# Kernel tuning notes

Hardware: AMD Instinct MI355X
Metric: run time of the kernel (lower is better)

Reference implementation:

```python
import jax, jax.numpy as jnp
import numpy as np

B, S, D = 4, 2048, 1024
H, DK, DV, DOUT = 16, 64, 64, 1024
NEG = -1.0e9


def setup_inputs() -> dict:
    key = jax.random.key(0)
    ks = jax.random.split(key, 12)
    sq = lambda fan_in: 1.0 / np.sqrt(fan_in)
    return {
        "query": jax.random.normal(ks[0], (B, S, D), jnp.float32),
        "key": jax.random.normal(ks[1], (B, S, D), jnp.float32),
        "value": jax.random.normal(ks[2], (B, S, D), jnp.float32),
        "attention_mask": jax.random.randint(ks[3], (B, 1, 1, S), 0, 2, jnp.int32),
        "wq": jax.random.normal(ks[4], (D, H * DK), jnp.float32) * sq(D),
        "bq": jnp.zeros((H * DK,), jnp.float32),
        "wk": jax.random.normal(ks[5], (D, H * DK), jnp.float32) * sq(D),
        "bk": jnp.zeros((H * DK,), jnp.float32),
        "wv": jax.random.normal(ks[6], (D, H * DV), jnp.float32) * sq(D),
        "bv": jnp.zeros((H * DV,), jnp.float32),
        "wo": jax.random.normal(ks[7], (H * DV, DOUT), jnp.float32) * sq(H * DV),
        "bo": jnp.zeros((DOUT,), jnp.float32),
    }


def _split_heads(x, head_dim):
    b, s, _ = x.shape
    return x.reshape(b, s, H, head_dim).transpose(0, 2, 1, 3)  # [B,H,S,hd]


def reference(query, key, value, attention_mask, wq, bq, wk, bk, wv, bv, wo, bo):
    q = _split_heads(query @ wq + bq, DK)   # [B,H,S,DK]
    k = _split_heads(key @ wk + bk, DK)     # [B,H,S,DK]
    v = _split_heads(value @ wv + bv, DV)   # [B,H,S,DV]
    logits = jnp.einsum("bhqd,bhkd->bhqk", q, k) / jnp.sqrt(jnp.float32(DK))
    logits = logits + attention_mask.astype(logits.dtype) * NEG
    attn = jax.nn.softmax(logits, axis=-1)
    out = jnp.einsum("bhqk,bhkd->bhqd", attn, v)          # [B,H,S,DV]
    out = out.transpose(0, 2, 1, 3).reshape(query.shape[0], -1, H * DV)
    return out @ wo + bo
```

## Files before the change

kernel.cpp:

```cpp
#include <hip/hip_runtime.h>
#include <hip/hip_bf16.h>
#include <math.h>

#define Bv 4
#define Sv 2048
#define Dv 1024
#define Hv 16
#define HD 64
#define NEGV (-1.0e9f)

typedef __attribute__((ext_vector_type(8))) short bf16x8;
typedef __attribute__((ext_vector_type(4))) short s16x4;
typedef __attribute__((ext_vector_type(4))) float f32x4;

__device__ __forceinline__ short f2bf(float f) {
    union { __hip_bfloat16 h; short s; } u;
    u.h = __float2bfloat16(f);
    return u.s;
}

__device__ __forceinline__ void glds16(const void* g, void* l) {
    __builtin_amdgcn_global_load_lds(
        (const __attribute__((address_space(1))) void*)g,
        (__attribute__((address_space(3))) void*)l, 16, 0, 0);
}

__global__ __launch_bounds__(256) void cvt_bf16(const float* __restrict__ X,
                                                unsigned short* __restrict__ Y) {
    const size_t i = ((size_t)blockIdx.x * 256 + threadIdx.x) * 8;
    const float4 a = *(const float4*)&X[i];
    const float4 b = *(const float4*)&X[i + 4];
    bf16x8 o = {f2bf(a.x), f2bf(a.y), f2bf(a.z), f2bf(a.w),
                f2bf(b.x), f2bf(b.y), f2bf(b.z), f2bf(b.w)};
    *(bf16x8*)&Y[i] = o;
}

__global__ __launch_bounds__(256) void transpose_w(const float* __restrict__ W,
                                                   unsigned short* __restrict__ WT) {
    __shared__ float T[64][65];
    const int t = threadIdx.x;
    const int n0 = blockIdx.x * 64, k0 = blockIdx.y * 64;
    #pragma unroll
    for (int i = 0; i < 4; ++i) {
        const int k = (t >> 4) + 16 * i;
        const int nc = (t & 15) * 4;
        const float4 v = *(const float4*)&W[(size_t)(k0 + k) * 1024 + n0 + nc];
        T[k][nc + 0] = v.x; T[k][nc + 1] = v.y;
        T[k][nc + 2] = v.z; T[k][nc + 3] = v.w;
    }
    __syncthreads();
    const int n = t >> 2, kc = (t & 3) * 16;
    #pragma unroll
    for (int j4 = 0; j4 < 4; ++j4) {
        s16x4 o;
        #pragma unroll
        for (int jj = 0; jj < 4; ++jj) o[jj] = f2bf(T[kc + j4 * 4 + jj][n]);
        *(s16x4*)&WT[(size_t)(n0 + n) * 1024 + k0 + kc + j4 * 4] = o;
    }
}

__global__ __launch_bounds__(256) void transpose_v(const unsigned short* __restrict__ Vin,
                                                   unsigned short* __restrict__ VT) {
    __shared__ unsigned short T[64][72];
    const int t = threadIdx.x;
    const int s0 = blockIdx.x * 64;
    const int bh = blockIdx.y;
    const size_t ib = (size_t)bh * Sv * 64;
    const size_t ob = (size_t)bh * 64 * Sv;
    {
        const int s = t >> 2, dc = (t & 3) * 16;
        const bf16x8 a = *(const bf16x8*)&Vin[ib + (size_t)(s0 + s) * 64 + dc];
        const bf16x8 b = *(const bf16x8*)&Vin[ib + (size_t)(s0 + s) * 64 + dc + 8];
        *(bf16x8*)&T[s][dc] = a;
        *(bf16x8*)&T[s][dc + 8] = b;
    }
    __syncthreads();
    const int dv = t >> 2, sc = (t & 3) * 16;
    #pragma unroll
    for (int j4 = 0; j4 < 4; ++j4) {
        s16x4 o;
        #pragma unroll
        for (int jj = 0; jj < 4; ++jj) o[jj] = (short)T[sc + j4 * 4 + jj][dv];
        *(s16x4*)&VT[ob + (size_t)dv * Sv + s0 + sc + j4 * 4] = o;
    }
}

template <int PERM>
__global__ __launch_bounds__(256) void gemm_mfma(const unsigned short* __restrict__ X,
                                                 const unsigned short* __restrict__ WT,
                                                 const float* __restrict__ bias,
                                                 void* __restrict__ Cv,
                                                 int M, int N, int K) {
    __shared__ short As[128 * 32];
    __shared__ short Bs[128 * 32];

    const int t = threadIdx.x;
    const int lane = t & 63, w = t >> 6;
    const int l15 = lane & 15, quad = lane >> 4;
    const int m0 = blockIdx.y * 128, n0 = blockIdx.x * 128;
    const int wm = (w >> 1) * 64, wn = (w & 1) * 64;

    f32x4 acc[4][4];
    #pragma unroll
    for (int mi = 0; mi < 4; ++mi)
        #pragma unroll
        for (int ni = 0; ni < 4; ++ni) acc[mi][ni] = (f32x4){0.f, 0.f, 0.f, 0.f};

    const int srow = lane >> 2;
    const int skc = (lane & 3) * 8;

    for (int k0 = 0; k0 < K; k0 += 32) {
        #pragma unroll
        for (int i = 0; i < 2; ++i) {
            const int seg = w * 2 + i;
            const int row = seg * 16 + srow;
            glds16(&WT[(size_t)(n0 + row) * K + k0 + skc], &Bs[seg * 512]);
            glds16(&X[(size_t)(m0 + row) * K + k0 + skc], &As[seg * 512]);
        }
        __syncthreads();

        bf16x8 afr[4], bfr[4];
        #pragma unroll
        for (int mi = 0; mi < 4; ++mi)
            afr[mi] = *(const bf16x8*)&As[(wm + mi * 16 + l15) * 32 + quad * 8];
        #pragma unroll
        for (int ni = 0; ni < 4; ++ni)
            bfr[ni] = *(const bf16x8*)&Bs[(wn + ni * 16 + l15) * 32 + quad * 8];
        #pragma unroll
        for (int mi = 0; mi < 4; ++mi)
            #pragma unroll
            for (int ni = 0; ni < 4; ++ni)
                acc[mi][ni] = __builtin_amdgcn_mfma_f32_16x16x32_bf16(
                    afr[mi], bfr[ni], acc[mi][ni], 0, 0, 0);
        __syncthreads();
    }

    #pragma unroll
    for (int mi = 0; mi < 4; ++mi) {
        #pragma unroll
        for (int ni = 0; ni < 4; ++ni) {
            const int col = n0 + wn + ni * 16 + l15;
            const float bsv = bias[col];
            #pragma unroll
            for (int r = 0; r < 4; ++r) {
                const int row = m0 + wm + mi * 16 + quad * 4 + r;
                const float vv = acc[mi][ni][r] + bsv;
                if constexpr (PERM == 0) {
                    ((float*)Cv)[(size_t)row * N + col] = vv;
                } else {
                    const int bb = row / Sv, s = row % Sv;
                    const int hh = col >> 6, d = col & 63;
                    ((unsigned short*)Cv)[((((size_t)bb * Hv + hh) * Sv + s) << 6) + d] =
                        (unsigned short)f2bf(vv);
                }
            }
        }
    }
}

__global__ __launch_bounds__(256) void attn_mfma(const unsigned short* __restrict__ Q,
                                                 const unsigned short* __restrict__ Kg,
                                                 const unsigned short* __restrict__ VT,
                                                 const int* __restrict__ mask,
                                                 unsigned short* __restrict__ O) {
    __shared__ short Kl[64 * 72];
    __shared__ short Vl[64 * 72];
    __shared__ short Sl[128 * 72];
    __shared__ float Mk[64];

    const int t = threadIdx.x;
    const int lane = t & 63, w = t >> 6;
    const int l15 = lane & 15, quad = lane >> 4;
    const int q0 = blockIdx.x * 128;
    const int h = blockIdx.y, b = blockIdx.z;
    const int bh = b * Hv + h;
    const size_t kvb = (size_t)bh * Sv * 64;
    const size_t vtb = (size_t)bh * 64 * Sv;

    bf16x8 qf[2][2];
    #pragma unroll
    for (int ni = 0; ni < 2; ++ni) {
        const size_t qa = kvb + (size_t)(q0 + w * 32 + ni * 16 + l15) * 64 + quad * 8;
        qf[ni][0] = *(const bf16x8*)&Q[qa];
        qf[ni][1] = *(const bf16x8*)&Q[qa + 32];
    }

    float l_acc[2] = {0.f, 0.f};
    f32x4 oacc[2][4];
    #pragma unroll
    for (int mi = 0; mi < 2; ++mi)
        #pragma unroll
        for (int ni = 0; ni < 4; ++ni) oacc[mi][ni] = (f32x4){0.f, 0.f, 0.f, 0.f};

    const int srow = t >> 2, sch = (t & 3) * 16;

    for (int k0 = 0; k0 < Sv; k0 += 64) {
        __syncthreads();
        {
            const unsigned short* Ks = Kg + kvb + (size_t)k0 * 64;
            const bf16x8 a = *(const bf16x8*)&Ks[(size_t)srow * 64 + sch];
            const bf16x8 c = *(const bf16x8*)&Ks[(size_t)srow * 64 + sch + 8];
            *(bf16x8*)&Kl[srow * 72 + sch] = a;
            *(bf16x8*)&Kl[srow * 72 + sch + 8] = c;
            const unsigned short* Vs = VT + vtb + k0;
            const bf16x8 d = *(const bf16x8*)&Vs[(size_t)srow * Sv + sch];
            const bf16x8 e = *(const bf16x8*)&Vs[(size_t)srow * Sv + sch + 8];
            *(bf16x8*)&Vl[srow * 72 + sch] = d;
            *(bf16x8*)&Vl[srow * 72 + sch + 8] = e;
        }
        if (t < 64) Mk[t] = NEGV * (float)mask[(size_t)b * Sv + k0 + t];
        __syncthreads();

        #pragma unroll
        for (int mi = 0; mi < 4; ++mi) {
            const bf16x8 kf0 = *(const bf16x8*)&Kl[(mi * 16 + l15) * 72 + quad * 8];
            const bf16x8 kf1 = *(const bf16x8*)&Kl[(mi * 16 + l15) * 72 + 32 + quad * 8];
            const float4 mk4 = *(const float4*)&Mk[mi * 16 + quad * 4];
            #pragma unroll
            for (int ni = 0; ni < 2; ++ni) {
                f32x4 st = (f32x4){0.f, 0.f, 0.f, 0.f};
                st = __builtin_amdgcn_mfma_f32_16x16x32_bf16(kf0, qf[ni][0], st, 0, 0, 0);
                st = __builtin_amdgcn_mfma_f32_16x16x32_bf16(kf1, qf[ni][1], st, 0, 0, 0);
                const float p0 = __expf(st[0] * 0.125f + mk4.x);
                const float p1 = __expf(st[1] * 0.125f + mk4.y);
                const float p2 = __expf(st[2] * 0.125f + mk4.z);
                const float p3 = __expf(st[3] * 0.125f + mk4.w);
                l_acc[ni] += (p0 + p1) + (p2 + p3);
                s16x4 pv = {f2bf(p0), f2bf(p1), f2bf(p2), f2bf(p3)};
                *(s16x4*)&Sl[(w * 32 + ni * 16 + l15) * 72 + mi * 16 + quad * 4] = pv;
            }
        }

        #pragma unroll
        for (int mi = 0; mi < 2; ++mi) {
            const bf16x8 pf0 = *(const bf16x8*)&Sl[(w * 32 + mi * 16 + l15) * 72 + quad * 8];
            const bf16x8 pf1 = *(const bf16x8*)&Sl[(w * 32 + mi * 16 + l15) * 72 + 32 + quad * 8];
            #pragma unroll
            for (int ni = 0; ni < 4; ++ni) {
                const bf16x8 vf0 = *(const bf16x8*)&Vl[(ni * 16 + l15) * 72 + quad * 8];
                const bf16x8 vf1 = *(const bf16x8*)&Vl[(ni * 16 + l15) * 72 + 32 + quad * 8];
                oacc[mi][ni] = __builtin_amdgcn_mfma_f32_16x16x32_bf16(pf0, vf0, oacc[mi][ni], 0, 0, 0);
                oacc[mi][ni] = __builtin_amdgcn_mfma_f32_16x16x32_bf16(pf1, vf1, oacc[mi][ni], 0, 0, 0);
            }
        }
    }

    #pragma unroll
    for (int mi = 0; mi < 2; ++mi) {
        float l = l_acc[mi];
        l += __shfl_xor(l, 16);
        l += __shfl_xor(l, 32);
        #pragma unroll
        for (int r = 0; r < 4; ++r) {
            const float lr = __shfl(l, quad * 4 + r, 64);
            const float inv = 1.0f / lr;
            const size_t row = (size_t)b * Sv + q0 + w * 32 + mi * 16 + quad * 4 + r;
            #pragma unroll
            for (int ni = 0; ni < 4; ++ni) {
                O[row * (Hv * HD) + h * HD + ni * 16 + l15] =
                    (unsigned short)f2bf(oacc[mi][ni][r] * inv);
            }
        }
    }
}

extern "C" void kernel_launch(void* const* d_in, const int* in_sizes, int n_in,
                              void* d_out, int out_size, void* d_ws, size_t ws_size,
                              hipStream_t stream) {
    const float* query = (const float*)d_in[0];
    const float* key   = (const float*)d_in[1];
    const float* value = (const float*)d_in[2];
    const int*   amask = (const int*)d_in[3];
    const float* wq = (const float*)d_in[4];
    const float* bq = (const float*)d_in[5];
    const float* wk = (const float*)d_in[6];
    const float* bk = (const float*)d_in[7];
    const float* wv = (const float*)d_in[8];
    const float* bv = (const float*)d_in[9];
    const float* wo = (const float*)d_in[10];
    const float* bo = (const float*)d_in[11];
    float* out = (float*)d_out;

    unsigned short* wsp = (unsigned short*)d_ws;
    dim3 bb(256), gt(16, 16);

    if (ws_size >= (size_t)64 * 1024 * 1024) {
        const size_t PBQ = (size_t)Bv * Hv * Sv * HD;
        unsigned short* qb = wsp;
        unsigned short* kb = qb + PBQ;
        unsigned short* vb = kb + PBQ;
        unsigned short* ab = vb + PBQ;
        unsigned short* wt_kb = kb;
        unsigned short* wt_out = (unsigned short*)d_out;
        unsigned short* wt_vb = vb;

        const int M = Bv * Sv;
        dim3 gg(8, M / 128), gc(M * 1024 / 2048);

        cvt_bf16<<<gc, bb, 0, stream>>>(value, ab);
        transpose_w<<<gt, bb, 0, stream>>>(wv, wt_kb);
        gemm_mfma<1><<<gg, bb, 0, stream>>>(ab, wt_kb, bv, qb, M, 1024, 1024);
        transpose_v<<<dim3(Sv / 64, Bv * Hv), bb, 0, stream>>>(qb, vb);

        cvt_bf16<<<gc, bb, 0, stream>>>(query, ab);
        transpose_w<<<gt, bb, 0, stream>>>(wq, wt_kb);
        gemm_mfma<1><<<gg, bb, 0, stream>>>(ab, wt_kb, bq, qb, M, 1024, 1024);

        cvt_bf16<<<gc, bb, 0, stream>>>(key, ab);
        transpose_w<<<gt, bb, 0, stream>>>(wk, wt_out);
        gemm_mfma<1><<<gg, bb, 0, stream>>>(ab, wt_out, bk, kb, M, 1024, 1024);

        attn_mfma<<<dim3(Sv / 128, Hv, Bv), bb, 0, stream>>>(qb, kb, vb, amask, ab);

        transpose_w<<<gt, bb, 0, stream>>>(wo, wt_vb);
        gemm_mfma<0><<<gg, bb, 0, stream>>>(ab, wt_vb, bo, out, M, 1024, 1024);
    } else {
        const size_t PQ = (size_t)Hv * Sv * HD;
        unsigned short* qb = wsp;
        unsigned short* kb = qb + PQ;
        unsigned short* vb = kb + PQ;
        unsigned short* ab = vb + PQ;
        const int M = Sv;
        dim3 gg(8, M / 128), gc(M * 1024 / 2048);
        for (int b = 0; b < Bv; ++b) {
            const size_t xoff = (size_t)b * Sv * Dv;
            unsigned short* wt_kb = kb;
            unsigned short* wt_out = (unsigned short*)(out + xoff);
            unsigned short* wt_vb = vb;

            cvt_bf16<<<gc, bb, 0, stream>>>(value + xoff, ab);
            transpose_w<<<gt, bb, 0, stream>>>(wv, wt_kb);
            gemm_mfma<1><<<gg, bb, 0, stream>>>(ab, wt_kb, bv, qb, M, 1024, 1024);
            transpose_v<<<dim3(Sv / 64, Hv), bb, 0, stream>>>(qb, vb);

            cvt_bf16<<<gc, bb, 0, stream>>>(query + xoff, ab);
            transpose_w<<<gt, bb, 0, stream>>>(wq, wt_kb);
            gemm_mfma<1><<<gg, bb, 0, stream>>>(ab, wt_kb, bq, qb, M, 1024, 1024);

            cvt_bf16<<<gc, bb, 0, stream>>>(key + xoff, ab);
            transpose_w<<<gt, bb, 0, stream>>>(wk, wt_out);
            gemm_mfma<1><<<gg, bb, 0, stream>>>(ab, wt_out, bk, kb, M, 1024, 1024);

            attn_mfma<<<dim3(Sv / 128, Hv, 1), bb, 0, stream>>>(qb, kb, vb,
                                                                amask + (size_t)b * Sv, ab);

            transpose_w<<<gt, bb, 0, stream>>>(wo, wt_vb);
            gemm_mfma<0><<<gg, bb, 0, stream>>>(ab, wt_vb, bo, out + xoff, M, 1024, 1024);
        }
    }
}
```

Before: 412.1 us.

## Register-prefetch next K/V/mask tile and use exp2 with folded scale in attention

The attention kernel now loads the next K, V and mask tile into registers right after the barrier, so the global-load latency overlaps the current tile's MFMA and softmax work. The softmax exponent uses a hardware exp2 with the 1/sqrt(dk)*log2(e) scale and the mask constant folded into a single FMA. The V fragments are hoisted out of the inner loop so each is read from LDS once. A launch-bounds occupancy hint of four blocks is added. The prefetch registers add register pressure, which the occupancy hint may conflict with.

```diff
diff --git a/kernel.cpp b/kernel.cpp
--- a/kernel.cpp
+++ b/kernel.cpp
@@ -18,6 +18,12 @@
     u.h = __float2bfloat16(f);
     return u.s;
 }
+
+#if __has_builtin(__builtin_amdgcn_exp2f)
+#define EXP2F(x) __builtin_amdgcn_exp2f(x)
+#else
+#define EXP2F(x) __expf((x) * 0.6931471805599453f)
+#endif
 
 __device__ __forceinline__ void glds16(const void* g, void* l) {
     __builtin_amdgcn_global_load_lds(
@@ -158,11 +164,11 @@
     }
 }
 
-__global__ __launch_bounds__(256) void attn_mfma(const unsigned short* __restrict__ Q,
-                                                 const unsigned short* __restrict__ Kg,
-                                                 const unsigned short* __restrict__ VT,
-                                                 const int* __restrict__ mask,
-                                                 unsigned short* __restrict__ O) {
+__global__ __launch_bounds__(256, 4) void attn_mfma(const unsigned short* __restrict__ Q,
+                                                    const unsigned short* __restrict__ Kg,
+                                                    const unsigned short* __restrict__ VT,
+                                                    const int* __restrict__ mask,
+                                                    unsigned short* __restrict__ O) {
     __shared__ short Kl[64 * 72];
     __shared__ short Vl[64 * 72];
     __shared__ short Sl[128 * 72];
@@ -193,23 +199,35 @@
         for (int ni = 0; ni < 4; ++ni) oacc[mi][ni] = (f32x4){0.f, 0.f, 0.f, 0.f};
 
     const int srow = t >> 2, sch = (t & 3) * 16;
+    const unsigned short* Kst = Kg + kvb + (size_t)srow * 64 + sch;
+    const unsigned short* Vst = VT + vtb + (size_t)srow * Sv + sch;
+    const int* Mst = mask + (size_t)b * Sv;
+
+    bf16x8 kr0 = *(const bf16x8*)&Kst[0];
+    bf16x8 kr1 = *(const bf16x8*)&Kst[8];
+    bf16x8 vr0 = *(const bf16x8*)&Vst[0];
+    bf16x8 vr1 = *(const bf16x8*)&Vst[8];
+    int mreg = (t < 64) ? Mst[t] : 0;
+
+    constexpr float CS = 0.18033688011112042f;
+    constexpr float CM = NEGV * 1.4426950408889634f;
 
     for (int k0 = 0; k0 < Sv; k0 += 64) {
         __syncthreads();
-        {
-            const unsigned short* Ks = Kg + kvb + (size_t)k0 * 64;
-            const bf16x8 a = *(const bf16x8*)&Ks[(size_t)srow * 64 + sch];
-            const bf16x8 c = *(const bf16x8*)&Ks[(size_t)srow * 64 + sch + 8];
-            *(bf16x8*)&Kl[srow * 72 + sch] = a;
-            *(bf16x8*)&Kl[srow * 72 + sch + 8] = c;
-            const unsigned short* Vs = VT + vtb + k0;
-            const bf16x8 d = *(const bf16x8*)&Vs[(size_t)srow * Sv + sch];
-            const bf16x8 e = *(const bf16x8*)&Vs[(size_t)srow * Sv + sch + 8];
-            *(bf16x8*)&Vl[srow * 72 + sch] = d;
-            *(bf16x8*)&Vl[srow * 72 + sch + 8] = e;
-        }
-        if (t < 64) Mk[t] = NEGV * (float)mask[(size_t)b * Sv + k0 + t];
+        *(bf16x8*)&Kl[srow * 72 + sch] = kr0;
+        *(bf16x8*)&Kl[srow * 72 + sch + 8] = kr1;
+        *(bf16x8*)&Vl[srow * 72 + sch] = vr0;
+        *(bf16x8*)&Vl[srow * 72 + sch + 8] = vr1;
+        if (t < 64) Mk[t] = CM * (float)mreg;
         __syncthreads();
+
+        if (k0 + 64 < Sv) {
+            kr0 = *(const bf16x8*)&Kst[(size_t)(k0 + 64) * 64];
+            kr1 = *(const bf16x8*)&Kst[(size_t)(k0 + 64) * 64 + 8];
+            vr0 = *(const bf16x8*)&Vst[k0 + 64];
+            vr1 = *(const bf16x8*)&Vst[k0 + 64 + 8];
+            if (t < 64) mreg = Mst[k0 + 64 + t];
+        }
 
         #pragma unroll
         for (int mi = 0; mi < 4; ++mi) {
@@ -221,26 +239,31 @@
                 f32x4 st = (f32x4){0.f, 0.f, 0.f, 0.f};
                 st = __builtin_amdgcn_mfma_f32_16x16x32_bf16(kf0, qf[ni][0], st, 0, 0, 0);
                 st = __builtin_amdgcn_mfma_f32_16x16x32_bf16(kf1, qf[ni][1], st, 0, 0, 0);
-                const float p0 = __expf(st[0] * 0.125f + mk4.x);
-                const float p1 = __expf(st[1] * 0.125f + mk4.y);
-                const float p2 = __expf(st[2] * 0.125f + mk4.z);
-                const float p3 = __expf(st[3] * 0.125f + mk4.w);
+                const float p0 = EXP2F(__builtin_fmaf(st[0], CS, mk4.x));
+                const float p1 = EXP2F(__builtin_fmaf(st[1], CS, mk4.y));
+                const float p2 = EXP2F(__builtin_fmaf(st[2], CS, mk4.z));
+                const float p3 = EXP2F(__builtin_fmaf(st[3], CS, mk4.w));
                 l_acc[ni] += (p0 + p1) + (p2 + p3);
                 s16x4 pv = {f2bf(p0), f2bf(p1), f2bf(p2), f2bf(p3)};
                 *(s16x4*)&Sl[(w * 32 + ni * 16 + l15) * 72 + mi * 16 + quad * 4] = pv;
             }
         }
 
+        bf16x8 vf[4][2];
+        #pragma unroll
+        for (int ni = 0; ni < 4; ++ni) {
+            vf[ni][0] = *(const bf16x8*)&Vl[(ni * 16 + l15) * 72 + quad * 8];
+            vf[ni][1] = *(const bf16x8*)&Vl[(ni * 16 + l15) * 72 + 32 + quad * 8];
+        }
+
         #pragma unroll
         for (int mi = 0; mi < 2; ++mi) {
             const bf16x8 pf0 = *(const bf16x8*)&Sl[(w * 32 + mi * 16 + l15) * 72 + quad * 8];
             const bf16x8 pf1 = *(const bf16x8*)&Sl[(w * 32 + mi * 16 + l15) * 72 + 32 + quad * 8];
             #pragma unroll
             for (int ni = 0; ni < 4; ++ni) {
-                const bf16x8 vf0 = *(const bf16x8*)&Vl[(ni * 16 + l15) * 72 + quad * 8];
-                const bf16x8 vf1 = *(const bf16x8*)&Vl[(ni * 16 + l15) * 72 + 32 + quad * 8];
-                oacc[mi][ni] = __builtin_amdgcn_mfma_f32_16x16x32_bf16(pf0, vf0, oacc[mi][ni], 0, 0, 0);
-                oacc[mi][ni] = __builtin_amdgcn_mfma_f32_16x16x32_bf16(pf1, vf1, oacc[mi][ni], 0, 0, 0);
+                oacc[mi][ni] = __builtin_amdgcn_mfma_f32_16x16x32_bf16(pf0, vf[ni][0], oacc[mi][ni], 0, 0, 0);
+                oacc[mi][ni] = __builtin_amdgcn_mfma_f32_16x16x32_bf16(pf1, vf[ni][1], oacc[mi][ni], 0, 0, 0);
             }
         }
     }
```

Measured after the change: 412.4 us. About the same (+0.1%).
